# Performance work log

Hardware: AMD Instinct MI355X
Metric: run time of the kernel (lower is better)

## Reference

```python
import jax, jax.numpy as jnp
import numpy as np

B, HID, NUM_RIS = 65536, 256, 64
R = NUM_RIS // 4  # number of 4-qubit circuit runs


def _cnot_perm(c, t):
    # basis index i has wire 0 as most-significant bit (matches shape (2,2,2,2) row-major)
    idx = np.arange(16)
    cbit = (idx >> (3 - c)) & 1
    return idx ^ (cbit << (3 - t))

P01 = jnp.asarray(_cnot_perm(0, 1))
P23 = jnp.asarray(_cnot_perm(2, 3))
P12 = jnp.asarray(_cnot_perm(1, 2))
P30 = jnp.asarray(_cnot_perm(3, 0))


def apply_ry(state, theta, wire):
    # state: (B, R, 2,2,2,2); theta broadcastable to (B, R)
    ax = 2 + wire
    c = jnp.cos(theta * 0.5)[..., None, None, None]
    s = jnp.sin(theta * 0.5)[..., None, None, None]
    s0 = jnp.take(state, 0, axis=ax)
    s1 = jnp.take(state, 1, axis=ax)
    return jnp.stack([c * s0 - s * s1, s * s0 + c * s1], axis=ax)


def apply_cnot(state, perm):
    b, r = state.shape[:2]
    return state.reshape(b, r, 16)[:, :, perm].reshape(b, r, 2, 2, 2, 2)


def setup_inputs() -> dict:
    key = jax.random.key(0)
    k1, k2, k3 = jax.random.split(key, 3)
    fused = jax.random.normal(k1, (B, HID), dtype=jnp.float32)
    W_proj = jax.random.normal(k2, (4 * R, HID), dtype=jnp.float32) * (1.0 / np.sqrt(HID))
    b_proj = jnp.zeros((4 * R,), dtype=jnp.float32)
    vqc_weights = jax.random.normal(k3, (R, 4, 4), dtype=jnp.float32) * 0.01
    return {"fused": fused, "W_proj": W_proj, "b_proj": b_proj, "vqc_weights": vqc_weights}


def reference(fused, W_proj, b_proj, vqc_weights):
    b = fused.shape[0]
    r = vqc_weights.shape[0]
    angles = jnp.tanh(fused @ W_proj.T + b_proj) * jnp.pi  # (B, 4R)
    angles = angles.reshape(b, r, 4)

    # initial |0000> state, batched over (B, R)
    state = jnp.zeros((b, r, 2, 2, 2, 2), dtype=fused.dtype).at[:, :, 0, 0, 0, 0].set(1.0)

    # input encoding layer
    for w in range(4):
        state = apply_ry(state, angles[:, :, w], w)
    # variational layer 0 + entanglers
    for w in range(4):
        state = apply_ry(state, vqc_weights[:, 0, w][None], w)
    state = apply_cnot(state, P01)
    state = apply_cnot(state, P23)
    # layer 1
    for w in range(4):
        state = apply_ry(state, vqc_weights[:, 1, w][None], w)
    state = apply_cnot(state, P12)
    state = apply_cnot(state, P30)
    # layer 2
    for w in range(4):
        state = apply_ry(state, vqc_weights[:, 2, w][None], w)
    state = apply_cnot(state, P01)
    state = apply_cnot(state, P12)
    state = apply_cnot(state, P23)
    state = apply_cnot(state, P30)
    # layer 3
    for w in range(4):
        state = apply_ry(state, vqc_weights[:, 3, w][None], w)

    # <Z_w> = sum(p | bit_w=0) - sum(p | bit_w=1)
    prob = state * state  # RY/CNOT keep state real
    evs = []
    for w in range(4):
        ax = 2 + w
        diff = jnp.take(prob, 0, axis=ax) - jnp.take(prob, 1, axis=ax)
        evs.append(diff.sum(axis=(2, 3, 4)))  # (B, R)
    z = jnp.stack(evs, axis=-1).reshape(b, r * 4)  # matches torch.cat over runs
    return (z + 1.0) * jnp.pi
```

## Files before the change

kernel.cpp:

```cpp
#include <hip/hip_runtime.h>
#include <math.h>


#define PI_F 3.14159265358979323846f

typedef _Float16 f16x4 __attribute__((ext_vector_type(4)));
typedef _Float16 f16x8 __attribute__((ext_vector_type(8)));
typedef float    f32x4 __attribute__((ext_vector_type(4)));
typedef float    f32x16 __attribute__((ext_vector_type(16)));

__device__ __forceinline__ void ry_gate(float st[16], float c, float s, int w) {
    const int m = 1 << (3 - w);
    #pragma unroll
    for (int i = 0; i < 16; ++i) {
        if (i & m) continue;
        float a = st[i];
        float b = st[i | m];
        st[i]     = c * a - s * b;
        st[i | m] = s * a + c * b;
    }
}

__device__ __forceinline__ void cnot_gate(float st[16], int cw, int tw) {
    const int cm = 1 << (3 - cw);
    const int tm = 1 << (3 - tw);
    #pragma unroll
    for (int i = 0; i < 16; ++i) {
        if ((i & cm) && !(i & tm)) {
            float tmp = st[i];
            st[i] = st[i | tm];
            st[i | tm] = tmp;
        }
    }
}

__global__ void prep_kernel(const float* __restrict__ vw,
                            const float* __restrict__ W,
                            char* __restrict__ ws) {
    const int tid = threadIdx.x;
    if (blockIdx.x == 0) {
        float* Ut = (float*)(ws + 49152);
        {
            const int r = tid >> 4, j = tid & 15;
            const float* wr = vw + r * 16;
            float cs[16], sn[16];
            #pragma unroll
            for (int i = 0; i < 16; ++i) {
                float h = wr[i] * 0.5f;
                cs[i] = __cosf(h);
                sn[i] = __sinf(h);
            }
            float st[16];
            #pragma unroll
            for (int i = 0; i < 16; ++i) st[i] = 0.f;
            st[j] = 1.f;
            #pragma unroll
            for (int w = 0; w < 4; ++w) ry_gate(st, cs[w], sn[w], w);
            cnot_gate(st, 0, 1);
            cnot_gate(st, 2, 3);
            #pragma unroll
            for (int w = 0; w < 4; ++w) ry_gate(st, cs[4 + w], sn[4 + w], w);
            cnot_gate(st, 1, 2);
            cnot_gate(st, 3, 0);
            #pragma unroll
            for (int w = 0; w < 4; ++w) ry_gate(st, cs[8 + w], sn[8 + w], w);
            cnot_gate(st, 0, 1);
            cnot_gate(st, 1, 2);
            cnot_gate(st, 2, 3);
            cnot_gate(st, 3, 0);
            #pragma unroll
            for (int w = 0; w < 4; ++w) ry_gate(st, cs[12 + w], sn[12 + w], w);
            #pragma unroll
            for (int i = 0; i < 16; ++i) Ut[r * 256 + i * 16 + j] = st[i];
        }
        __syncthreads();
        {
            _Float16* UA = (_Float16*)(ws + 32768);
            #pragma unroll
            for (int t = 0; t < 4; ++t) {
                int f = t * 256 + tid;
                int r = f >> 6, lane = f & 63;
                int i = lane & 31, hh = lane >> 5;
                const float* urow = Ut + r * 256 + (i & 15) * 16;
                f16x8 h;
                #pragma unroll
                for (int e = 0; e < 8; ++e) {
                    float u = urow[8 * hh + e];
                    if (i < 16) {
                        h[e] = (_Float16)u;
                    } else {
                        _Float16 hi = (_Float16)u;
                        h[e] = (_Float16)(u - (float)hi);
                    }
                }
                *(f16x8*)(UA + f * 8) = h;
            }
        }
    } else {
        _Float16* Wh = (_Float16*)ws;
        #pragma unroll
        for (int t = 0; t < 8; ++t) {
            int f  = tid * 8 + t;
            int cg = f >> 9;
            int kk = (f >> 6) & 7;
            int l  = f & 63;
            int row = cg * 16 + (l & 15);
            int k0  = (kk * 4 + (l >> 4)) * 8;
            const float* src = W + row * 256 + k0;
            f16x8 h;
            #pragma unroll
            for (int e = 0; e < 8; ++e) h[e] = (_Float16)src[e];
            *(f16x8*)(Wh + f * 8) = h;
        }
    }
}

__global__ __launch_bounds__(256, 5) void vqc_main_kernel(
        const float* __restrict__ fused,
        const char* __restrict__ ws,
        const float* __restrict__ bp,
        float* __restrict__ out) {
    __shared__ __align__(16) char smem[16384];
    _Float16* tab = (_Float16*)smem;

    const int tid  = threadIdx.x;
    const int lane = tid & 63;
    const int cg   = tid >> 6;
    const int l15  = lane & 15;
    const int l4   = lane >> 4;
    const size_t b0 = (size_t)blockIdx.x * 32;

    float4 stg[8];
    {
        const float4* s4 = (const float4*)(fused + b0 * 256);
        #pragma unroll
        for (int it = 0; it < 8; ++it) stg[it] = s4[tid + it * 256];
    }

    const f16x8* Wf = (const f16x8*)ws;
    f16x8 af[8];
    #pragma unroll
    for (int kk = 0; kk < 8; ++kk) af[kk] = Wf[(cg * 8 + kk) * 64 + lane];

    float4 bb = *(const float4*)(bp + 4 * (4 * cg + l4));

    #pragma unroll
    for (int it = 0; it < 8; ++it) {
        int q = tid + it * 256;
        float4 v = stg[it];
        int row = q >> 6;
        int c4  = (q & 63) << 2;
        int sl  = (c4 >> 3) ^ (row & 7);
        int byteoff = row * 512 + (sl << 4) + ((c4 & 7) << 1);
        f16x4 h = { (_Float16)v.x, (_Float16)v.y, (_Float16)v.z, (_Float16)v.w };
        *(f16x4*)(smem + byteoff) = h;
    }
    __syncthreads();

    f32x4 acc[2] = {};
    #pragma unroll
    for (int kk = 0; kk < 8; ++kk) {
        int slot = kk * 4 + l4;
        #pragma unroll
        for (int sg = 0; sg < 2; ++sg) {
            int frow = sg * 16 + l15;
            f16x8 bf = *(const f16x8*)(smem + frow * 512 + ((slot ^ (frow & 7)) << 4));
            acc[sg] = __builtin_amdgcn_mfma_f32_16x16x32_f16(af[kk], bf, acc[sg], 0, 0, 0);
        }
    }
    __syncthreads();

    const int r_own = 4 * cg + l4;
    #pragma unroll
    for (int sg = 0; sg < 2; ++sg) {
        float bias[4] = {bb.x, bb.y, bb.z, bb.w};
        float cc[4], ssn[4];
        #pragma unroll
        for (int w = 0; w < 4; ++w) {
            float pre = acc[sg][w] + bias[w];
            float e   = __expf(2.f * pre);
            float th  = __fdividef(e - 1.f, e + 1.f);
            float ha  = th * (0.5f * PI_F);
            __sincosf(ha, &ssn[w], &cc[w]);
        }
        f16x8 tt;
        tt[0] = (_Float16)(cc[0] * cc[1]);  tt[1] = (_Float16)(cc[0] * ssn[1]);
        tt[2] = (_Float16)(ssn[0] * cc[1]); tt[3] = (_Float16)(ssn[0] * ssn[1]);
        tt[4] = (_Float16)(cc[2] * cc[3]);  tt[5] = (_Float16)(cc[2] * ssn[3]);
        tt[6] = (_Float16)(ssn[2] * cc[3]); tt[7] = (_Float16)(ssn[2] * ssn[3]);
        *(f16x8*)(tab + (r_own * 32 + sg * 16 + l15) * 8) = tt;
    }

    const f16x8* UA = (const f16x8*)(ws + 32768);
    const int   s32 = lane & 31;
    const int   hh  = lane >> 5;
    const float g1  = hh ? -1.f : 1.f;

    #pragma unroll
    for (int rr = 0; rr < 4; ++rr) {
        const int r = 4 * cg + rr;
        f16x8 ua = UA[r * 64 + lane];
        f16x8 tt = *(const f16x8*)(tab + (r * 32 + s32) * 8);
        _Float16 a0 = tt[2 * hh], a1 = tt[2 * hh + 1];
        f16x8 se;
        se[0] = a0 * tt[4]; se[1] = a0 * tt[5];
        se[2] = a0 * tt[6]; se[3] = a0 * tt[7];
        se[4] = a1 * tt[4]; se[5] = a1 * tt[5];
        se[6] = a1 * tt[6]; se[7] = a1 * tt[7];

        f32x16 zero = {};
        f32x16 o = __builtin_amdgcn_mfma_f32_32x32x16_f16(ua, se, zero, 0, 0, 0);

        float p[8];
        #pragma unroll
        for (int j = 0; j < 8; ++j) {
            float of = o[j] + o[j + 8];
            p[j] = of * of;
        }
        float a = p[0] + p[1], b = p[2] + p[3];
        float c = p[4] + p[5], d = p[6] + p[7];
        float ab = a + b, cd = c + d;
        float z0 = ab - cd;
        float z1 = g1 * (ab + cd);
        float z2 = (a - b) + (c - d);
        float z3 = (p[0] - p[1] + p[2] - p[3]) + (p[4] - p[5] + p[6] - p[7]);

        z0 += __shfl_xor(z0, 32);
        z1 += __shfl_xor(z1, 32);
        z2 += __shfl_xor(z2, 32);
        z3 += __shfl_xor(z3, 32);

        if (hh == 0) {
            float4 ov;
            ov.x = (z0 + 1.f) * PI_F;
            ov.y = (z1 + 1.f) * PI_F;
            ov.z = (z2 + 1.f) * PI_F;
            ov.w = (z3 + 1.f) * PI_F;
            *(float4*)(out + (b0 + s32) * 64 + 4 * r) = ov;
        }
    }
}

extern "C" void kernel_launch(void* const* d_in, const int* in_sizes, int n_in,
                              void* d_out, int out_size, void* d_ws, size_t ws_size,
                              hipStream_t stream) {
    const float* fused = (const float*)d_in[0];
    const float* Wp    = (const float*)d_in[1];
    const float* bp    = (const float*)d_in[2];
    const float* vw    = (const float*)d_in[3];
    float* out = (float*)d_out;
    char*  ws  = (char*)d_ws;

    prep_kernel<<<2, 256, 0, stream>>>(vw, Wp, ws);

    const int B = 65536;
    vqc_main_kernel<<<B / 32, 256, 0, stream>>>(fused, ws, bp, out);
}
```

Measured before the change: 27.46 us.

## Process two 32-row batch tiles per block to amortize weight fragment loads

Each block now handles 64 batch rows as two 32-row tiles. The W fragments, bias and U matrix loads are shared across both tiles, and each thread issues twice as many independent global loads up front. The grid is halved, and shared memory per block doubles to 32 KB. Launch bounds drop to 4 blocks per SM, so register pressure rises and occupancy falls.

```diff
diff --git a/kernel.cpp b/kernel.cpp
--- a/kernel.cpp
+++ b/kernel.cpp
@@ -115,12 +115,12 @@
     }
 }
 
-__global__ __launch_bounds__(256, 5) void vqc_main_kernel(
+__global__ __launch_bounds__(256, 4) void vqc_main_kernel(
         const float* __restrict__ fused,
         const char* __restrict__ ws,
         const float* __restrict__ bp,
         float* __restrict__ out) {
-    __shared__ __align__(16) char smem[16384];
+    __shared__ __align__(16) char smem[32768];
     _Float16* tab = (_Float16*)smem;
 
     const int tid  = threadIdx.x;
@@ -128,13 +128,15 @@
     const int cg   = tid >> 6;
     const int l15  = lane & 15;
     const int l4   = lane >> 4;
-    const size_t b0 = (size_t)blockIdx.x * 32;
-
-    float4 stg[8];
+    const size_t b0 = (size_t)blockIdx.x * 64;
+
+    float4 stg0[8], stg1[8];
     {
         const float4* s4 = (const float4*)(fused + b0 * 256);
         #pragma unroll
-        for (int it = 0; it < 8; ++it) stg[it] = s4[tid + it * 256];
+        for (int it = 0; it < 8; ++it) stg0[it] = s4[tid + it * 256];
+        #pragma unroll
+        for (int it = 0; it < 8; ++it) stg1[it] = s4[2048 + tid + it * 256];
     }
 
     const f16x8* Wf = (const f16x8*)ws;
@@ -147,48 +149,57 @@
     #pragma unroll
     for (int it = 0; it < 8; ++it) {
         int q = tid + it * 256;
-        float4 v = stg[it];
         int row = q >> 6;
         int c4  = (q & 63) << 2;
         int sl  = (c4 >> 3) ^ (row & 7);
         int byteoff = row * 512 + (sl << 4) + ((c4 & 7) << 1);
-        f16x4 h = { (_Float16)v.x, (_Float16)v.y, (_Float16)v.z, (_Float16)v.w };
-        *(f16x4*)(smem + byteoff) = h;
+        float4 v0 = stg0[it];
+        f16x4 h0 = { (_Float16)v0.x, (_Float16)v0.y, (_Float16)v0.z, (_Float16)v0.w };
+        *(f16x4*)(smem + byteoff) = h0;
+        float4 v1 = stg1[it];
+        f16x4 h1 = { (_Float16)v1.x, (_Float16)v1.y, (_Float16)v1.z, (_Float16)v1.w };
+        *(f16x4*)(smem + 16384 + byteoff) = h1;
     }
     __syncthreads();
 
-    f32x4 acc[2] = {};
+    f32x4 acc[2][2] = {};
     #pragma unroll
     for (int kk = 0; kk < 8; ++kk) {
         int slot = kk * 4 + l4;
         #pragma unroll
         for (int sg = 0; sg < 2; ++sg) {
             int frow = sg * 16 + l15;
-            f16x8 bf = *(const f16x8*)(smem + frow * 512 + ((slot ^ (frow & 7)) << 4));
-            acc[sg] = __builtin_amdgcn_mfma_f32_16x16x32_f16(af[kk], bf, acc[sg], 0, 0, 0);
+            int off  = frow * 512 + ((slot ^ (frow & 7)) << 4);
+            f16x8 bf0 = *(const f16x8*)(smem + off);
+            f16x8 bf1 = *(const f16x8*)(smem + 16384 + off);
+            acc[0][sg] = __builtin_amdgcn_mfma_f32_16x16x32_f16(af[kk], bf0, acc[0][sg], 0, 0, 0);
+            acc[1][sg] = __builtin_amdgcn_mfma_f32_16x16x32_f16(af[kk], bf1, acc[1][sg], 0, 0, 0);
         }
     }
     __syncthreads();
 
     const int r_own = 4 * cg + l4;
     #pragma unroll
-    for (int sg = 0; sg < 2; ++sg) {
-        float bias[4] = {bb.x, bb.y, bb.z, bb.w};
-        float cc[4], ssn[4];
-        #pragma unroll
-        for (int w = 0; w < 4; ++w) {
-            float pre = acc[sg][w] + bias[w];
-            float e   = __expf(2.f * pre);
-            float th  = __fdividef(e - 1.f, e + 1.f);
-            float ha  = th * (0.5f * PI_F);
-            __sincosf(ha, &ssn[w], &cc[w]);
-        }
-        f16x8 tt;
-        tt[0] = (_Float16)(cc[0] * cc[1]);  tt[1] = (_Float16)(cc[0] * ssn[1]);
-        tt[2] = (_Float16)(ssn[0] * cc[1]); tt[3] = (_Float16)(ssn[0] * ssn[1]);
-        tt[4] = (_Float16)(cc[2] * cc[3]);  tt[5] = (_Float16)(cc[2] * ssn[3]);
-        tt[6] = (_Float16)(ssn[2] * cc[3]); tt[7] = (_Float16)(ssn[2] * ssn[3]);
-        *(f16x8*)(tab + (r_own * 32 + sg * 16 + l15) * 8) = tt;
+    for (int tile = 0; tile < 2; ++tile) {
+        #pragma unroll
+        for (int sg = 0; sg < 2; ++sg) {
+            float bias[4] = {bb.x, bb.y, bb.z, bb.w};
+            float cc[4], ssn[4];
+            #pragma unroll
+            for (int w = 0; w < 4; ++w) {
+                float pre = acc[tile][sg][w] + bias[w];
+                float e   = __expf(2.f * pre);
+                float th  = __fdividef(e - 1.f, e + 1.f);
+                float ha  = th * (0.5f * PI_F);
+                __sincosf(ha, &ssn[w], &cc[w]);
+            }
+            f16x8 tt;
+            tt[0] = (_Float16)(cc[0] * cc[1]);  tt[1] = (_Float16)(cc[0] * ssn[1]);
+            tt[2] = (_Float16)(ssn[0] * cc[1]); tt[3] = (_Float16)(ssn[0] * ssn[1]);
+            tt[4] = (_Float16)(cc[2] * cc[3]);  tt[5] = (_Float16)(cc[2] * ssn[3]);
+            tt[6] = (_Float16)(ssn[2] * cc[3]); tt[7] = (_Float16)(ssn[2] * ssn[3]);
+            *(f16x8*)(tab + tile * 4096 + (r_own * 32 + sg * 16 + l15) * 8) = tt;
+        }
     }
 
     const f16x8* UA = (const f16x8*)(ws + 32768);
@@ -200,43 +211,46 @@
     for (int rr = 0; rr < 4; ++rr) {
         const int r = 4 * cg + rr;
         f16x8 ua = UA[r * 64 + lane];
-        f16x8 tt = *(const f16x8*)(tab + (r * 32 + s32) * 8);
-        _Float16 a0 = tt[2 * hh], a1 = tt[2 * hh + 1];
-        f16x8 se;
-        se[0] = a0 * tt[4]; se[1] = a0 * tt[5];
-        se[2] = a0 * tt[6]; se[3] = a0 * tt[7];
-        se[4] = a1 * tt[4]; se[5] = a1 * tt[5];
-        se[6] = a1 * tt[6]; se[7] = a1 * tt[7];
-
-        f32x16 zero = {};
-        f32x16 o = __builtin_amdgcn_mfma_f32_32x32x16_f16(ua, se, zero, 0, 0, 0);
-
-        float p[8];
-        #pragma unroll
-        for (int j = 0; j < 8; ++j) {
-            float of = o[j] + o[j + 8];
-            p[j] = of * of;
-        }
-        float a = p[0] + p[1], b = p[2] + p[3];
-        float c = p[4] + p[5], d = p[6] + p[7];
-        float ab = a + b, cd = c + d;
-        float z0 = ab - cd;
-        float z1 = g1 * (ab + cd);
-        float z2 = (a - b) + (c - d);
-        float z3 = (p[0] - p[1] + p[2] - p[3]) + (p[4] - p[5] + p[6] - p[7]);
-
-        z0 += __shfl_xor(z0, 32);
-        z1 += __shfl_xor(z1, 32);
-        z2 += __shfl_xor(z2, 32);
-        z3 += __shfl_xor(z3, 32);
-
-        if (hh == 0) {
-            float4 ov;
-            ov.x = (z0 + 1.f) * PI_F;
-            ov.y = (z1 + 1.f) * PI_F;
-            ov.z = (z2 + 1.f) * PI_F;
-            ov.w = (z3 + 1.f) * PI_F;
-            *(float4*)(out + (b0 + s32) * 64 + 4 * r) = ov;
+        #pragma unroll
+        for (int tile = 0; tile < 2; ++tile) {
+            f16x8 tt = *(const f16x8*)(tab + tile * 4096 + (r * 32 + s32) * 8);
+            _Float16 a0 = tt[2 * hh], a1 = tt[2 * hh + 1];
+            f16x8 se;
+            se[0] = a0 * tt[4]; se[1] = a0 * tt[5];
+            se[2] = a0 * tt[6]; se[3] = a0 * tt[7];
+            se[4] = a1 * tt[4]; se[5] = a1 * tt[5];
+            se[6] = a1 * tt[6]; se[7] = a1 * tt[7];
+
+            f32x16 zero = {};
+            f32x16 o = __builtin_amdgcn_mfma_f32_32x32x16_f16(ua, se, zero, 0, 0, 0);
+
+            float p[8];
+            #pragma unroll
+            for (int j = 0; j < 8; ++j) {
+                float of = o[j] + o[j + 8];
+                p[j] = of * of;
+            }
+            float a = p[0] + p[1], b = p[2] + p[3];
+            float c = p[4] + p[5], d = p[6] + p[7];
+            float ab = a + b, cd = c + d;
+            float z0 = ab - cd;
+            float z1 = g1 * (ab + cd);
+            float z2 = (a - b) + (c - d);
+            float z3 = (p[0] - p[1] + p[2] - p[3]) + (p[4] - p[5] + p[6] - p[7]);
+
+            z0 += __shfl_xor(z0, 32);
+            z1 += __shfl_xor(z1, 32);
+            z2 += __shfl_xor(z2, 32);
+            z3 += __shfl_xor(z3, 32);
+
+            if (hh == 0) {
+                float4 ov;
+                ov.x = (z0 + 1.f) * PI_F;
+                ov.y = (z1 + 1.f) * PI_F;
+                ov.z = (z2 + 1.f) * PI_F;
+                ov.w = (z3 + 1.f) * PI_F;
+                *(float4*)(out + (b0 + tile * 32 + s32) * 64 + 4 * r) = ov;
+            }
         }
     }
 }
@@ -254,5 +268,5 @@
     prep_kernel<<<2, 256, 0, stream>>>(vw, Wp, ws);
 
     const int B = 65536;
-    vqc_main_kernel<<<B / 32, 256, 0, stream>>>(fused, ws, bp, out);
-}
+    vqc_main_kernel<<<B / 64, 256, 0, stream>>>(fused, ws, bp, out);
+}
```

After: 29.33 us. 1.07x slower.
